# Kernel tuning notes

Measured on AMD Instinct MI355X. Metric: run time of the kernel, lower is better.

Reference implementation:

```python
import jax, jax.numpy as jnp
import numpy as np
from jax import lax

DIM = 512
E = 16
NC = 1000
ROUTER_TEMP = 1.0


def _conv(x, w, b):
    # NCHW conv, 3x3, SAME padding (matches nn.Conv2d(padding=1))
    y = lax.conv_general_dilated(x, w, (1, 1), 'SAME',
                                 dimension_numbers=('NCHW', 'OIHW', 'NCHW'))
    return y + b[None, :, None, None]


def _avgpool2(x):
    B, C, H, W = x.shape
    return x.reshape(B, C, H // 2, 2, W // 2, 2).mean(axis=(3, 5))


def setup_inputs() -> dict:
    key = jax.random.key(0)
    ks = jax.random.split(key, 12)
    B, C, H, W = 128, 3, 128, 128

    def init(k, shape, fan_in):
        return jax.random.normal(k, shape, jnp.float32) * (1.0 / np.sqrt(fan_in))

    return {
        'x': jax.random.normal(ks[0], (B, C, H, W), jnp.float32),
        'conv1_w': init(ks[1], (32, 3, 3, 3), 3 * 9),   'conv1_b': jnp.zeros((32,), jnp.float32),
        'conv2_w': init(ks[2], (32, 32, 3, 3), 32 * 9), 'conv2_b': jnp.zeros((32,), jnp.float32),
        'conv3_w': init(ks[3], (64, 32, 3, 3), 32 * 9), 'conv3_b': jnp.zeros((64,), jnp.float32),
        'conv4_w': init(ks[4], (64, 64, 3, 3), 64 * 9), 'conv4_b': jnp.zeros((64,), jnp.float32),
        'proj_w': init(ks[5], (64, DIM), 64),           'proj_b': jnp.zeros((DIM,), jnp.float32),
        'router_w': init(ks[6], (DIM, E), DIM),         'router_b': jnp.zeros((E,), jnp.float32),
        # stacked expert MLPs: Linear(dim,dim) -> ReLU -> Linear(dim,num_classes)
        'w1': init(ks[7], (E, DIM, DIM), DIM), 'b1': jnp.zeros((E, DIM), jnp.float32),
        'w2': init(ks[8], (E, DIM, NC), DIM),  'b2': jnp.zeros((E, NC), jnp.float32),
    }


def reference(x, conv1_w, conv1_b, conv2_w, conv2_b, conv3_w, conv3_b,
              conv4_w, conv4_b, proj_w, proj_b, router_w, router_b,
              w1, b1, w2, b2):
    # ---- Encoder ----
    h = jax.nn.relu(_conv(x, conv1_w, conv1_b))
    h = jax.nn.relu(_conv(h, conv2_w, conv2_b))
    h = _avgpool2(h)
    h = jax.nn.relu(_conv(h, conv3_w, conv3_b))
    h = _avgpool2(h)
    h = jax.nn.relu(_conv(h, conv4_w, conv4_b))
    h = h.mean(axis=(2, 3))                      # AdaptiveAvgPool2d(1) -> [B, 64]
    z = h @ proj_w + proj_b                      # [B, DIM]

    # ---- Router (top-1 gating) ----
    gate_logits = (z @ router_w + router_b) / ROUTER_TEMP   # [B, E]
    gate_probs = jax.nn.softmax(gate_logits, axis=-1)
    top1 = jnp.argmax(gate_probs, axis=-1)                  # [B] int
    B = z.shape[0]

    counts = lax.stop_gradient(
        jnp.zeros((E,), jnp.float32).at[top1].add(1.0) / B)
    importance = gate_probs.mean(axis=0)                    # [E]
    aux_loss = E * jnp.sum(counts * importance)

    # ---- Expert dispatch: gather per-token expert weights (top-1 hard routing) ----
    h1 = jax.nn.relu(jnp.einsum('bd,bdk->bk', z, w1[top1]) + b1[top1])   # [B, DIM]
    logits = jnp.einsum('bd,bdk->bk', h1, w2[top1]) + b2[top1]           # [B, NC]

    return logits, aux_loss, lax.stop_gradient(counts), lax.stop_gradient(importance)
```

## Files before the change

kernel.cpp:

```cpp
#include <hip/hip_runtime.h>
#include <math.h>

typedef unsigned short ushort_t;
typedef short short4x __attribute__((ext_vector_type(4)));
typedef short short8 __attribute__((ext_vector_type(8)));
typedef float f32x16 __attribute__((ext_vector_type(16)));

#define MFMA32(A,B,C) __builtin_amdgcn_mfma_f32_32x32x16_bf16(A,B,C,0,0,0)

__device__ __forceinline__ ushort_t f2bf(float f) {
    union { float f; unsigned u; } c; c.f = f;
    unsigned u = c.u;
    unsigned r = (u + 0x7FFFu + ((u >> 16) & 1u)) >> 16;
    return (ushort_t)r;
}

__device__ __forceinline__ unsigned pk2bf(float lo, float hi) {
    unsigned r;
    asm("v_cvt_pk_bf16_f32 %0, %1, %2" : "=v"(r) : "v"(lo), "v"(hi));
    return r;
}

__global__ __launch_bounds__(256) void k_wcvt(
    const float* __restrict__ c1w, const float* __restrict__ c2w,
    const float* __restrict__ c3w, const float* __restrict__ c4w,
    ushort_t* __restrict__ c1f, ushort_t* __restrict__ w2f,
    ushort_t* __restrict__ w3f, ushort_t* __restrict__ w4f,
    float* __restrict__ feat, float* __restrict__ tail)
{
    if (blockIdx.x == 33) {
        for (int i = threadIdx.x; i < 8192; i += 256) feat[i] = 0.f;
        if (threadIdx.x < 33) tail[threadIdx.x] = 0.f;
        return;
    }
    int r = blockIdx.x * 256 + threadIdx.x;
    int lane = r & 63, m = lane & 31, g = (lane >> 5) & 1;
    if (r < 1152) {
        int f = r >> 6, tau = f >> 1, h = f & 1, ky = tau / 3, kx = tau % 3;
        #pragma unroll
        for (int j = 0; j < 8; ++j) {
            int ic = h * 16 + g * 8 + j;
            w2f[r * 8 + j] = f2bf(c2w[((m * 32 + ic) * 3 + ky) * 3 + kx]);
        }
    } else if (r < 3456) {
        int rr = r - 1152;
        int f = rr >> 6;
        int ot = f / 18, fl = f % 18, tau = fl >> 1, h = fl & 1, ky = tau / 3, kx = tau % 3;
        int oc = ot * 32 + m;
        #pragma unroll
        for (int j = 0; j < 8; ++j) {
            int ic = h * 16 + g * 8 + j;
            w3f[rr * 8 + j] = f2bf(c3w[((oc * 32 + ic) * 3 + ky) * 3 + kx]);
        }
    } else if (r < 8064) {
        int rr = r - 3456;
        int f = rr >> 6;
        int ot = f / 36, fl = f % 36, tau = fl >> 2, h = fl & 3, ky = tau / 3, kx = tau % 3;
        int oc = ot * 32 + m;
        #pragma unroll
        for (int j = 0; j < 8; ++j) {
            int ic = h * 16 + g * 8 + j;
            w4f[rr * 8 + j] = f2bf(c4w[((oc * 64 + ic) * 3 + ky) * 3 + kx]);
        }
    } else if (r < 8256) {
        int rr = r - 8064;
        int f = rr >> 6;
        #pragma unroll
        for (int j = 0; j < 8; ++j) {
            int k = f * 16 + g * 8 + j;
            int p = k >> 2, c = k & 3;
            ushort_t v = 0;
            if (p < 9 && c < 3)
                v = f2bf(c1w[(m * 3 + c) * 9 + p]);
            c1f[rr * 8 + j] = v;
        }
    }
}

__global__ __launch_bounds__(512, 4) void k_c12(
    const float* __restrict__ x,
    const ushort_t* __restrict__ c1f, const float* __restrict__ c1b,
    const ushort_t* __restrict__ w2f, const float* __restrict__ c2b,
    ushort_t* __restrict__ a2, int zoff)
{
    __shared__ __align__(16) ushort_t xs[1600];
    __shared__ __align__(16) ushort_t a1s[324 * 40];
    __shared__ float c2bs[32], c1bs[32];
    const int t = threadIdx.x;
    const int bx = blockIdx.x, by = blockIdx.y, b = blockIdx.z + zoff;
    const int ox0 = bx * 16, oy0 = by * 16;

    if (t < 32) { c2bs[t] = c2b[t]; c1bs[t] = c1b[t]; }
    for (int i = t; i < 400; i += 512) {
        int yy = i / 20, xx = i % 20;
        int gy = oy0 - 2 + yy, gx = ox0 - 2 + xx;
        float v0 = 0.f, v1 = 0.f, v2 = 0.f;
        if (gy >= 0 && gy < 128 && gx >= 0 && gx < 128) {
            const float* px = x + ((size_t)(b * 3) * 128 + gy) * 128 + gx;
            v0 = px[0]; v1 = px[16384]; v2 = px[32768];
        }
        uint2 pk;
        pk.x = pk2bf(v0, v1);
        pk.y = pk2bf(v2, 0.f);
        *(uint2*)&xs[i * 4] = pk;
    }

    const int wave = t >> 6, lane = t & 63;
    const int n = lane & 31, g = lane >> 5;

    short8 a1f0 = *(const short8*)(c1f + lane * 8);
    short8 a1f1 = *(const short8*)(c1f + (64 + lane) * 8);
    short8 a1f2 = *(const short8*)(c1f + (128 + lane) * 8);
    __syncthreads();

    float cb1[16];
    #pragma unroll
    for (int qd = 0; qd < 4; ++qd)
        #pragma unroll
        for (int jj = 0; jj < 4; ++jj)
            cb1[qd * 4 + jj] = c1bs[qd * 8 + 4 * g + jj];

    for (int grp = wave; grp < 11; grp += 8) {
        int q = grp * 32 + n;
        bool qv = q < 324;
        int qc = qv ? q : 0;
        int cy = qc / 18, cx = qc % 18;
        int gy = oy0 - 1 + cy, gx = ox0 - 1 + cx;
        bool inimg = qv && gy >= 0 && gy < 128 && gx >= 0 && gx < 128;
        int base = (cy * 20 + cx) * 4;

        short4x q0 = *(const short4x*)&xs[base + (g ? 8 : 0)];
        short4x q1 = *(const short4x*)&xs[base + (g ? 80 : 4)];
        short4x q2 = *(const short4x*)&xs[base + (g ? 160 : 84)];
        short4x q3 = *(const short4x*)&xs[base + (g ? 164 : 88)];
        short4x q4 = *(const short4x*)&xs[base + 168];

        short8 b0 = __builtin_shufflevector(q0, q1, 0, 1, 2, 3, 4, 5, 6, 7);
        short8 b1 = __builtin_shufflevector(q2, q3, 0, 1, 2, 3, 4, 5, 6, 7);
        short8 b2 = __builtin_shufflevector(q4, q4, 0, 1, 2, 3, 0, 1, 2, 3);

        f32x16 acc;
        #pragma unroll
        for (int i = 0; i < 16; ++i) acc[i] = 0.f;
        acc = MFMA32(a1f0, b0, acc);
        acc = MFMA32(a1f1, b1, acc);
        acc = MFMA32(a1f2, b2, acc);

        if (qv) {
            ushort_t* dst = &a1s[q * 40 + 4 * g];
            #pragma unroll
            for (int qd = 0; qd < 4; ++qd) {
                float v0 = fmaxf(acc[qd * 4 + 0] + cb1[qd * 4 + 0], 0.f);
                float v1 = fmaxf(acc[qd * 4 + 1] + cb1[qd * 4 + 1], 0.f);
                float v2 = fmaxf(acc[qd * 4 + 2] + cb1[qd * 4 + 2], 0.f);
                float v3 = fmaxf(acc[qd * 4 + 3] + cb1[qd * 4 + 3], 0.f);
                uint2 pk;
                pk.x = inimg ? pk2bf(v0, v1) : 0u;
                pk.y = inimg ? pk2bf(v2, v3) : 0u;
                *(uint2*)&dst[8 * qd] = pk;
            }
        }
    }
    __syncthreads();

    const int ry = n >> 4, rx = n & 15;
    const int y2 = wave * 2 + ry;

    short8 af[18];
    #pragma unroll
    for (int f = 0; f < 18; ++f)
        af[f] = *(const short8*)(w2f + (f * 64 + lane) * 8);

    f32x16 acc;
    #pragma unroll
    for (int i = 0; i < 16; ++i) acc[i] = 0.f;

    #pragma unroll
    for (int tau = 0; tau < 9; ++tau) {
        int dy = tau / 3, dx = tau % 3;
        const ushort_t* bb = &a1s[((y2 + dy) * 18 + (rx + dx)) * 40 + g * 8];
        short8 b0 = *(const short8*)(bb);
        short8 b1 = *(const short8*)(bb + 16);
        acc = MFMA32(af[tau * 2 + 0], b0, acc);
        acc = MFMA32(af[tau * 2 + 1], b1, acc);
    }

    const int opy = by * 8 + wave;
    const int opx = bx * 8 + (rx >> 1);
    float pv[16];
    #pragma unroll
    for (int r = 0; r < 16; ++r) {
        float v = fmaxf(acc[r] + c2bs[(r & 3) + 8 * (r >> 2) + 4 * g], 0.f);
        v += __shfl_xor(v, 1);
        v += __shfl_xor(v, 16);
        pv[r] = v * 0.25f;
    }
    if ((lane & 17) == 0) {
        ushort_t* dst = &a2[(((size_t)b * 64 + opy) * 64 + opx) * 32 + 4 * g];
        #pragma unroll
        for (int qd = 0; qd < 4; ++qd) {
            uint2 pk;
            pk.x = pk2bf(pv[qd * 4 + 0], pv[qd * 4 + 1]);
            pk.y = pk2bf(pv[qd * 4 + 2], pv[qd * 4 + 3]);
            *(uint2*)&dst[8 * qd] = pk;
        }
    }
}

__global__ __launch_bounds__(512, 4) void k_c3(
    const ushort_t* __restrict__ a2, const ushort_t* __restrict__ w3f,
    const float* __restrict__ c3b, ushort_t* __restrict__ a3)
{
    __shared__ __align__(16) ushort_t s[324 * 40];
    __shared__ float bs[64];
    const int t = threadIdx.x;
    const int bx = blockIdx.x, by = blockIdx.y, b = blockIdx.z;
    const int x0 = bx * 16, y0 = by * 16;
    if (t < 64) bs[t] = c3b[t];
    for (int idx = t; idx < 1296; idx += 512) {
        int cell = idx >> 2, part = idx & 3;
        int cy = cell / 18, cx = cell % 18;
        int gy = y0 - 1 + cy, gx = x0 - 1 + cx;
        uint4 v = make_uint4(0, 0, 0, 0);
        if (gy >= 0 && gy < 64 && gx >= 0 && gx < 64)
            v = *(const uint4*)(a2 + (((size_t)b * 64 + gy) * 64 + gx) * 32 + part * 8);
        *(uint4*)(&s[cell * 40 + part * 8]) = v;
    }
    __syncthreads();

    const int wave = t >> 6, lane = t & 63;
    const int n = lane & 31, g = lane >> 5;
    const int ry = n >> 4, rx = n & 15;
    const int y3 = wave * 2 + ry;

    f32x16 acc0, acc1;
    #pragma unroll
    for (int i = 0; i < 16; ++i) { acc0[i] = 0.f; acc1[i] = 0.f; }

    #pragma unroll
    for (int tau = 0; tau < 9; ++tau) {
        int dy = tau / 3, dx = tau % 3;
        const ushort_t* bb = &s[((y3 + dy) * 18 + (rx + dx)) * 40 + g * 8];
        short8 b0 = *(const short8*)(bb);
        short8 b1 = *(const short8*)(bb + 16);
        short8 a00 = *(const short8*)(w3f + ((tau * 2 + 0) * 64 + lane) * 8);
        short8 a01 = *(const short8*)(w3f + ((tau * 2 + 1) * 64 + lane) * 8);
        short8 a10 = *(const short8*)(w3f + (((18 + tau * 2) + 0) * 64 + lane) * 8);
        short8 a11 = *(const short8*)(w3f + (((18 + tau * 2) + 1) * 64 + lane) * 8);
        acc0 = MFMA32(a00, b0, acc0);
        acc0 = MFMA32(a01, b1, acc0);
        acc1 = MFMA32(a10, b0, acc1);
        acc1 = MFMA32(a11, b1, acc1);
    }

    const int opy = by * 8 + wave;
    const int opx = bx * 8 + (rx >> 1);
    ushort_t* dst = &a3[(((size_t)b * 32 + opy) * 32 + opx) * 64 + 4 * g];
    #pragma unroll
    for (int ot = 0; ot < 2; ++ot) {
        const f32x16& ac = ot ? acc1 : acc0;
        float pv[16];
        #pragma unroll
        for (int r = 0; r < 16; ++r) {
            float v = fmaxf(ac[r] + bs[ot * 32 + (r & 3) + 8 * (r >> 2) + 4 * g], 0.f);
            v += __shfl_xor(v, 1);
            v += __shfl_xor(v, 16);
            pv[r] = v * 0.25f;
        }
        if ((lane & 17) == 0) {
            #pragma unroll
            for (int qd = 0; qd < 4; ++qd) {
                uint2 pk;
                pk.x = pk2bf(pv[qd * 4 + 0], pv[qd * 4 + 1]);
                pk.y = pk2bf(pv[qd * 4 + 2], pv[qd * 4 + 3]);
                *(uint2*)&dst[ot * 32 + 8 * qd] = pk;
            }
        }
    }
}

__global__ __launch_bounds__(512, 2) void k_c4(
    const ushort_t* __restrict__ a3, const ushort_t* __restrict__ w4f,
    const float* __restrict__ c4b, float* __restrict__ feat)
{
    __shared__ __align__(16) ushort_t s[324 * 72];
    __shared__ float bs[64];
    const int t = threadIdx.x;
    const int bx = blockIdx.x, by = blockIdx.y, b = blockIdx.z;
    const int x0 = bx * 16, y0 = by * 16;
    if (t < 64) bs[t] = c4b[t];
    for (int idx = t; idx < 2592; idx += 512) {
        int cell = idx >> 3, part = idx & 7;
        int cy = cell / 18, cx = cell % 18;
        int gy = y0 - 1 + cy, gx = x0 - 1 + cx;
        uint4 v = make_uint4(0, 0, 0, 0);
        if (gy >= 0 && gy < 32 && gx >= 0 && gx < 32)
            v = *(const uint4*)(a3 + (((size_t)b * 32 + gy) * 32 + gx) * 64 + part * 8);
        *(uint4*)(&s[cell * 72 + part * 8]) = v;
    }
    __syncthreads();

    const int wave = t >> 6, lane = t & 63;
    const int n = lane & 31, g = lane >> 5;
    const int ry = n >> 4, rx = n & 15;
    const int y4 = wave * 2 + ry;

    f32x16 acc0, acc1;
    #pragma unroll
    for (int i = 0; i < 16; ++i) { acc0[i] = 0.f; acc1[i] = 0.f; }

    #pragma unroll
    for (int hp = 0; hp < 2; ++hp) {
        #pragma unroll
        for (int tau = 0; tau < 9; ++tau) {
            int dy = tau / 3, dx = tau % 3;
            const ushort_t* bb = &s[((y4 + dy) * 18 + (rx + dx)) * 72 + hp * 32 + g * 8];
            short8 b0 = *(const short8*)(bb);
            short8 b1 = *(const short8*)(bb + 16);
            short8 a00 = *(const short8*)(w4f + ((tau * 4 + hp * 2 + 0) * 64 + lane) * 8);
            short8 a01 = *(const short8*)(w4f + ((tau * 4 + hp * 2 + 1) * 64 + lane) * 8);
            short8 a10 = *(const short8*)(w4f + ((36 + tau * 4 + hp * 2 + 0) * 64 + lane) * 8);
            short8 a11 = *(const short8*)(w4f + ((36 + tau * 4 + hp * 2 + 1) * 64 + lane) * 8);
            acc0 = MFMA32(a00, b0, acc0);
            acc0 = MFMA32(a01, b1, acc0);
            acc1 = MFMA32(a10, b0, acc1);
            acc1 = MFMA32(a11, b1, acc1);
        }
    }

    #pragma unroll
    for (int ot = 0; ot < 2; ++ot) {
        const f32x16& ac = ot ? acc1 : acc0;
        #pragma unroll
        for (int r = 0; r < 16; ++r) {
            int oc = ot * 32 + (r & 3) + 8 * (r >> 2) + 4 * g;
            float v = fmaxf(ac[r] + bs[oc], 0.f);
            v += __shfl_xor(v, 1);
            v += __shfl_xor(v, 2);
            v += __shfl_xor(v, 4);
            v += __shfl_xor(v, 8);
            v += __shfl_xor(v, 16);
            if ((lane & 31) == 0)
                atomicAdd(&feat[b * 64 + oc], v * (1.0f / 1024.0f));
        }
    }
}

__global__ __launch_bounds__(256) void k_router(
    const float* __restrict__ meanacc,
    const float* __restrict__ pw, const float* __restrict__ pb,
    const float* __restrict__ rw, const float* __restrict__ rb,
    ushort_t* __restrict__ zb, int* __restrict__ top1, float* __restrict__ tail)
{
    __shared__ float m[64];
    __shared__ float zs[512];
    __shared__ float part[256];
    __shared__ float gate[16];
    const int b = blockIdx.x, t = threadIdx.x;
    if (t < 64) m[t] = meanacc[b * 64 + t];
    __syncthreads();

    #pragma unroll
    for (int j = 0; j < 2; ++j) {
        int d = t + j * 256;
        float s = pb[d];
        for (int c = 0; c < 64; ++c) s += m[c] * pw[c * 512 + d];
        zs[d] = s;
        zb[b * 512 + d] = f2bf(s);
    }
    __syncthreads();
    {
        int e = t & 15, gg = t >> 4;
        float s = 0.f;
        for (int j = 0; j < 32; ++j) {
            int d = gg * 32 + j;
            s += zs[d] * rw[d * 16 + e];
        }
        part[t] = s;
    }
    __syncthreads();
    if (t < 16) {
        float s = rb[t];
        for (int gg = 0; gg < 16; ++gg) s += part[gg * 16 + t];
        gate[t] = s;
    }
    __syncthreads();
    if (t == 0) {
        float mx = gate[0];
        int am = 0;
        for (int e = 1; e < 16; ++e)
            if (gate[e] > mx) { mx = gate[e]; am = e; }
        float pr[16];
        float sum = 0.f;
        for (int e = 0; e < 16; ++e) { pr[e] = expf(gate[e] - mx); sum += pr[e]; }
        float inv = 1.f / sum;
        top1[b] = am;
        atomicAdd(&tail[1 + am], 1.0f / 128.0f);
        for (int e = 0; e < 16; ++e)
            atomicAdd(&tail[17 + e], pr[e] * inv * (1.0f / 128.0f));
    }
}

__global__ void k_sort(const int* __restrict__ top1, int* __restrict__ meta,
                       int* __restrict__ perm, float* __restrict__ tail)
{
    __shared__ int c[16], o[16], pos[128];
    const int t = threadIdx.x;
    if (t < 16) c[t] = 0;
    __syncthreads();
    int e = 0;
    if (t < 128) { e = top1[t]; pos[t] = atomicAdd(&c[e], 1); }
    __syncthreads();
    if (t == 0) {
        int s = 0;
        for (int i = 0; i < 16; ++i) { o[i] = s; s += c[i]; }
        int nt = 0;
        for (int i = 0; i < 16; ++i) {
            for (int r0 = 0; r0 < c[i]; r0 += 32) {
                meta[33 + nt] = i;
                meta[53 + nt] = o[i] + r0;
                int rem = c[i] - r0;
                meta[73 + nt] = rem < 32 ? rem : 32;
                ++nt;
            }
        }
        meta[32] = nt;
        for (int k = nt; k < 20; ++k) { meta[33 + k] = 0; meta[53 + k] = 0; meta[73 + k] = 0; }
        float s2 = 0.f;
        for (int i = 0; i < 16; ++i) s2 += tail[1 + i] * tail[17 + i];
        tail[0] = 16.0f * s2;
    }
    __syncthreads();
    if (t < 128) perm[o[e] + pos[t]] = t;
    if (t < 16) { meta[t] = c[t]; meta[16 + t] = o[t]; }
}

__global__ __launch_bounds__(64) void k_mlp1(
    const ushort_t* __restrict__ zb, const int* __restrict__ meta, const int* __restrict__ perm,
    const float* __restrict__ w1, const float* __restrict__ b1, ushort_t* __restrict__ h1b)
{
    const int ty = blockIdx.y;
    if (ty >= meta[32]) return;
    const int e = meta[33 + ty], ts = meta[53 + ty], rows = meta[73 + ty];
    const int n0 = blockIdx.x * 32;
    __shared__ __align__(16) ushort_t ws[32 * 520];
    __shared__ int tks[32];
    const int lane = threadIdx.x;
    const int mn = lane & 31, g = lane >> 5;

    if (lane < 32) tks[lane] = (lane < rows) ? perm[ts + lane] : -1;

    const float* Wg = w1 + ((size_t)e << 18) + n0;
    {
        const int cq = lane & 7, dg = lane >> 3;
        #pragma unroll 4
        for (int it = 0; it < 32; ++it) {
            int d = it * 16 + dg * 2;
            float4 va = *(const float4*)(Wg + (size_t)d * 512 + 4 * cq);
            float4 vb = *(const float4*)(Wg + (size_t)(d + 1) * 512 + 4 * cq);
            *(unsigned*)&ws[(4 * cq + 0) * 520 + d] = pk2bf(va.x, vb.x);
            *(unsigned*)&ws[(4 * cq + 1) * 520 + d] = pk2bf(va.y, vb.y);
            *(unsigned*)&ws[(4 * cq + 2) * 520 + d] = pk2bf(va.z, vb.z);
            *(unsigned*)&ws[(4 * cq + 3) * 520 + d] = pk2bf(va.w, vb.w);
        }
    }
    __syncthreads();

    const int tok_a = tks[mn] < 0 ? 0 : tks[mn];
    const ushort_t* za = zb + (size_t)tok_a * 512;

    f32x16 acc;
    #pragma unroll
    for (int i = 0; i < 16; ++i) acc[i] = 0.f;

    #pragma unroll 4
    for (int kt = 0; kt < 16; ++kt) {
        int k0 = kt * 32;
        short8 a0 = *(const short8*)(za + k0 + g * 8);
        short8 a1 = *(const short8*)(za + k0 + 16 + g * 8);
        short8 b0 = *(const short8*)(&ws[mn * 520 + k0 + g * 8]);
        short8 b1 = *(const short8*)(&ws[mn * 520 + k0 + 16 + g * 8]);
        acc = MFMA32(a0, b0, acc);
        acc = MFMA32(a1, b1, acc);
    }

    const float bias = b1[e * 512 + n0 + mn];
    #pragma unroll
    for (int r = 0; r < 16; ++r) {
        int mrow = (r & 3) + 8 * (r >> 2) + 4 * g;
        int tok = tks[mrow];
        if (tok >= 0) {
            float v = fmaxf(acc[r] + bias, 0.f);
            h1b[(size_t)tok * 512 + n0 + mn] = f2bf(v);
        }
    }
}

__global__ __launch_bounds__(64) void k_mlp2(
    const ushort_t* __restrict__ h1b, const int* __restrict__ meta, const int* __restrict__ perm,
    const float* __restrict__ w2, const float* __restrict__ b2, float* __restrict__ out)
{
    const int ty = blockIdx.y;
    if (ty >= meta[32]) return;
    const int e = meta[33 + ty], ts = meta[53 + ty], rows = meta[73 + ty];
    const int n0 = blockIdx.x * 32;
    __shared__ __align__(16) ushort_t ws[32 * 520];
    __shared__ int tks[32];
    const int lane = threadIdx.x;
    const int mn = lane & 31, g = lane >> 5;

    if (lane < 32) tks[lane] = (lane < rows) ? perm[ts + lane] : -1;

    const float* Wg = w2 + (size_t)e * 512000 + n0;
    {
        const int cq = lane & 7, dg = lane >> 3;
        const bool cut = (n0 == 992) && (cq >= 2);
        #pragma unroll 4
        for (int it = 0; it < 32; ++it) {
            int d = it * 16 + dg * 2;
            float4 va = make_float4(0.f, 0.f, 0.f, 0.f), vb = va;
            if (!cut) {
                va = *(const float4*)(Wg + (size_t)d * 1000 + 4 * cq);
                vb = *(const float4*)(Wg + (size_t)(d + 1) * 1000 + 4 * cq);
            }
            *(unsigned*)&ws[(4 * cq + 0) * 520 + d] = pk2bf(va.x, vb.x);
            *(unsigned*)&ws[(4 * cq + 1) * 520 + d] = pk2bf(va.y, vb.y);
            *(unsigned*)&ws[(4 * cq + 2) * 520 + d] = pk2bf(va.z, vb.z);
            *(unsigned*)&ws[(4 * cq + 3) * 520 + d] = pk2bf(va.w, vb.w);
        }
    }
    __syncthreads();

    const int tok_a = tks[mn] < 0 ? 0 : tks[mn];
    const ushort_t* ha = h1b + (size_t)tok_a * 512;

    f32x16 acc;
    #pragma unroll
    for (int i = 0; i < 16; ++i) acc[i] = 0.f;

    #pragma unroll 4
    for (int kt = 0; kt < 16; ++kt) {
        int k0 = kt * 32;
        short8 a0 = *(const short8*)(ha + k0 + g * 8);
        short8 a1 = *(const short8*)(ha + k0 + 16 + g * 8);
        short8 b0 = *(const short8*)(&ws[mn * 520 + k0 + g * 8]);
        short8 b1 = *(const short8*)(&ws[mn * 520 + k0 + 16 + g * 8]);
        acc = MFMA32(a0, b0, acc);
        acc = MFMA32(a1, b1, acc);
    }

    const int col = n0 + mn;
    if (col < 1000) {
        const float bias = b2[e * 1000 + col];
        #pragma unroll
        for (int r = 0; r < 16; ++r) {
            int mrow = (r & 3) + 8 * (r >> 2) + 4 * g;
            int tok = tks[mrow];
            if (tok >= 0)
                out[(size_t)tok * 1000 + col] = acc[r] + bias;
        }
    }
}

extern "C" void kernel_launch(void* const* d_in, const int* in_sizes, int n_in,
                              void* d_out, int out_size, void* d_ws, size_t ws_size,
                              hipStream_t stream)
{
    const float* x   = (const float*)d_in[0];
    const float* c1w = (const float*)d_in[1];
    const float* c1b = (const float*)d_in[2];
    const float* c2w = (const float*)d_in[3];
    const float* c2b = (const float*)d_in[4];
    const float* c3w = (const float*)d_in[5];
    const float* c3b = (const float*)d_in[6];
    const float* c4w = (const float*)d_in[7];
    const float* c4b = (const float*)d_in[8];
    const float* pw  = (const float*)d_in[9];
    const float* pb  = (const float*)d_in[10];
    const float* rw  = (const float*)d_in[11];
    const float* rb  = (const float*)d_in[12];
    const float* w1  = (const float*)d_in[13];
    const float* b1  = (const float*)d_in[14];
    const float* w2  = (const float*)d_in[15];
    const float* b2  = (const float*)d_in[16];

    float* out = (float*)d_out;
    float* tail = out + 128000;

    char* w = (char*)d_ws;
    ushort_t* a2   = (ushort_t*)(w);
    ushort_t* a3   = (ushort_t*)(w + 33554432);
    ushort_t* w2f  = (ushort_t*)(w + 50331648);
    ushort_t* w3f  = (ushort_t*)(w + 50350080);
    ushort_t* w4f  = (ushort_t*)(w + 50386944);
    ushort_t* c1f  = (ushort_t*)(w + 50460672);
    float*    feat = (float*)(w + 50464768);
    ushort_t* zb   = (ushort_t*)(w + 50497536);
    ushort_t* h1b  = (ushort_t*)(w + 50628608);
    int*      top1 = (int*)(w + 50759680);
    int*      meta = (int*)(w + 50760192);
    int*      perm = (int*)(w + 50760704);

    k_wcvt  <<<34, 256, 0, stream>>>(c1w, c2w, c3w, c4w, c1f, w2f, w3f, w4f, feat, tail);
    k_c12   <<<dim3(8, 8, 64), 512, 0, stream>>>(x, c1f, c1b, w2f, c2b, a2, 0);
    k_c12   <<<dim3(8, 8, 64), 512, 0, stream>>>(x, c1f, c1b, w2f, c2b, a2, 64);
    k_c3    <<<dim3(4, 4, 128), 512, 0, stream>>>(a2, w3f, c3b, a3);
    k_c4    <<<dim3(2, 2, 128), 512, 0, stream>>>(a3, w4f, c4b, feat);
    k_router<<<128, 256, 0, stream>>>(feat, pw, pb, rw, rb, zb, top1, tail);
    k_sort  <<<1, 128, 0, stream>>>(top1, meta, perm, tail);
    k_mlp1  <<<dim3(16, 20), 64, 0, stream>>>(zb, meta, perm, w1, b1, h1b);
    k_mlp2  <<<dim3(32, 20), 64, 0, stream>>>(h1b, meta, perm, w2, b2, out);
}
```

Measured before the change: 206.1 us.

## Switch conv2-4 to 16x16x32 MFMA with pool-grouped pixel mapping

Reworks the conv2, conv3 and conv4 inner loops to use the 16x16x32 bf16 MFMA with activations as the A operand and repacked weights as B. Rows are mapped so each group of four rows is one 2x2 pooling window, which lets pooling be done in registers without cross-lane shuffles. Conv4 now reduces into shared memory before a single global atomic per channel, and its occupancy bound is raised from 2 to 4. The two half-batch conv1/2 launches are merged into one. The trade-off is more MFMA instructions with fewer cycles each, plus narrower per-element global stores.

```diff
diff --git a/kernel.cpp b/kernel.cpp
--- a/kernel.cpp
+++ b/kernel.cpp
@@ -4,9 +4,11 @@
 typedef unsigned short ushort_t;
 typedef short short4x __attribute__((ext_vector_type(4)));
 typedef short short8 __attribute__((ext_vector_type(8)));
+typedef float f32x4 __attribute__((ext_vector_type(4)));
 typedef float f32x16 __attribute__((ext_vector_type(16)));
 
 #define MFMA32(A,B,C) __builtin_amdgcn_mfma_f32_32x32x16_bf16(A,B,C,0,0,0)
+#define MFMA16(A,B,C) __builtin_amdgcn_mfma_f32_16x16x32_bf16(A,B,C,0,0,0)
 
 __device__ __forceinline__ ushort_t f2bf(float f) {
     union { float f; unsigned u; } c; c.f = f;
@@ -34,40 +36,41 @@
         return;
     }
     int r = blockIdx.x * 256 + threadIdx.x;
-    int lane = r & 63, m = lane & 31, g = (lane >> 5) & 1;
-    if (r < 1152) {
-        int f = r >> 6, tau = f >> 1, h = f & 1, ky = tau / 3, kx = tau % 3;
+    int f = r >> 6, lane = r & 63;
+    int col = lane & 15, kg = lane >> 4;
+    if (f < 18) {
+        int tau = f >> 1, ocg = f & 1;
+        int oc = ocg * 16 + col;
         #pragma unroll
         for (int j = 0; j < 8; ++j) {
-            int ic = h * 16 + g * 8 + j;
-            w2f[r * 8 + j] = f2bf(c2w[((m * 32 + ic) * 3 + ky) * 3 + kx]);
-        }
-    } else if (r < 3456) {
-        int rr = r - 1152;
-        int f = rr >> 6;
-        int ot = f / 18, fl = f % 18, tau = fl >> 1, h = fl & 1, ky = tau / 3, kx = tau % 3;
-        int oc = ot * 32 + m;
+            int ic = kg * 8 + j;
+            w2f[r * 8 + j] = f2bf(c2w[(oc * 32 + ic) * 9 + tau]);
+        }
+    } else if (f < 54) {
+        int rr = f - 18;
+        int tau = rr >> 2, ocg = rr & 3;
+        int oc = ocg * 16 + col;
         #pragma unroll
         for (int j = 0; j < 8; ++j) {
-            int ic = h * 16 + g * 8 + j;
-            w3f[rr * 8 + j] = f2bf(c3w[((oc * 32 + ic) * 3 + ky) * 3 + kx]);
-        }
-    } else if (r < 8064) {
-        int rr = r - 3456;
-        int f = rr >> 6;
-        int ot = f / 36, fl = f % 36, tau = fl >> 2, h = fl & 3, ky = tau / 3, kx = tau % 3;
-        int oc = ot * 32 + m;
+            int ic = kg * 8 + j;
+            w3f[(r - 18 * 64) * 8 + j] = f2bf(c3w[(oc * 32 + ic) * 9 + tau]);
+        }
+    } else if (f < 126) {
+        int rr = f - 54;
+        int q = rr >> 2, ocg = rr & 3, tau = q >> 1, ks = q & 1;
+        int oc = ocg * 16 + col;
         #pragma unroll
         for (int j = 0; j < 8; ++j) {
-            int ic = h * 16 + g * 8 + j;
-            w4f[rr * 8 + j] = f2bf(c4w[((oc * 64 + ic) * 3 + ky) * 3 + kx]);
-        }
-    } else if (r < 8256) {
-        int rr = r - 8064;
-        int f = rr >> 6;
+            int ic = ks * 32 + kg * 8 + j;
+            w4f[(r - 54 * 64) * 8 + j] = f2bf(c4w[(oc * 64 + ic) * 9 + tau]);
+        }
+    } else if (f < 129) {
+        int rr = r - 126 * 64;
+        int f1 = rr >> 6;
+        int m = lane & 31, g = (lane >> 5) & 1;
         #pragma unroll
         for (int j = 0; j < 8; ++j) {
-            int k = f * 16 + g * 8 + j;
+            int k = f1 * 16 + g * 8 + j;
             int p = k >> 2, c = k & 3;
             ushort_t v = 0;
             if (p < 9 && c < 3)
@@ -81,13 +84,13 @@
     const float* __restrict__ x,
     const ushort_t* __restrict__ c1f, const float* __restrict__ c1b,
     const ushort_t* __restrict__ w2f, const float* __restrict__ c2b,
-    ushort_t* __restrict__ a2, int zoff)
+    ushort_t* __restrict__ a2)
 {
     __shared__ __align__(16) ushort_t xs[1600];
     __shared__ __align__(16) ushort_t a1s[324 * 40];
     __shared__ float c2bs[32], c1bs[32];
     const int t = threadIdx.x;
-    const int bx = blockIdx.x, by = blockIdx.y, b = blockIdx.z + zoff;
+    const int bx = blockIdx.x, by = blockIdx.y, b = blockIdx.z;
     const int ox0 = bx * 16, oy0 = by * 16;
 
     if (t < 32) { c2bs[t] = c2b[t]; c1bs[t] = c1b[t]; }
@@ -163,47 +166,33 @@
     }
     __syncthreads();
 
-    const int ry = n >> 4, rx = n & 15;
-    const int y2 = wave * 2 + ry;
-
-    short8 af[18];
-    #pragma unroll
-    for (int f = 0; f < 18; ++f)
-        af[f] = *(const short8*)(w2f + (f * 64 + lane) * 8);
-
-    f32x16 acc;
-    #pragma unroll
-    for (int i = 0; i < 16; ++i) acc[i] = 0.f;
-
-    #pragma unroll
-    for (int tau = 0; tau < 9; ++tau) {
-        int dy = tau / 3, dx = tau % 3;
-        const ushort_t* bb = &a1s[((y2 + dy) * 18 + (rx + dx)) * 40 + g * 8];
-        short8 b0 = *(const short8*)(bb);
-        short8 b1 = *(const short8*)(bb + 16);
-        acc = MFMA32(af[tau * 2 + 0], b0, acc);
-        acc = MFMA32(af[tau * 2 + 1], b1, acc);
-    }
-
-    const int opy = by * 8 + wave;
-    const int opx = bx * 8 + (rx >> 1);
-    float pv[16];
-    #pragma unroll
-    for (int r = 0; r < 16; ++r) {
-        float v = fmaxf(acc[r] + c2bs[(r & 3) + 8 * (r >> 2) + 4 * g], 0.f);
-        v += __shfl_xor(v, 1);
-        v += __shfl_xor(v, 16);
-        pv[r] = v * 0.25f;
-    }
-    if ((lane & 17) == 0) {
-        ushort_t* dst = &a2[(((size_t)b * 64 + opy) * 64 + opx) * 32 + 4 * g];
-        #pragma unroll
-        for (int qd = 0; qd < 4; ++qd) {
-            uint2 pk;
-            pk.x = pk2bf(pv[qd * 4 + 0], pv[qd * 4 + 1]);
-            pk.y = pk2bf(pv[qd * 4 + 2], pv[qd * 4 + 3]);
-            *(uint2*)&dst[8 * qd] = pk;
-        }
+    const int col = lane & 15, kg = lane >> 4;
+    const float bias0 = c2bs[col], bias1 = c2bs[16 + col];
+    #pragma unroll
+    for (int i = 0; i < 2; ++i) {
+        const int pg = wave * 2 + i;
+        const int qiA = pg * 4 + (col >> 2), subA = col & 3;
+        const int y2 = (qiA >> 3) * 2 + (subA >> 1);
+        const int x2 = (qiA & 7) * 2 + (subA & 1);
+        const ushort_t* abase = &a1s[(y2 * 18 + x2) * 40 + kg * 8];
+        f32x4 acc0 = {0.f, 0.f, 0.f, 0.f}, acc1 = {0.f, 0.f, 0.f, 0.f};
+        #pragma unroll
+        for (int tau = 0; tau < 9; ++tau) {
+            short8 a = *(const short8*)(abase + ((tau / 3) * 18 + (tau % 3)) * 40);
+            short8 w0 = *(const short8*)(w2f + ((tau * 2 + 0) * 64 + lane) * 8);
+            short8 w1 = *(const short8*)(w2f + ((tau * 2 + 1) * 64 + lane) * 8);
+            acc0 = MFMA16(a, w0, acc0);
+            acc1 = MFMA16(a, w1, acc1);
+        }
+        const int qo = pg * 4 + kg;
+        const int poy = by * 8 + (qo >> 3), pox = bx * 8 + (qo & 7);
+        float s0 = fmaxf(acc0[0] + bias0, 0.f) + fmaxf(acc0[1] + bias0, 0.f)
+                 + fmaxf(acc0[2] + bias0, 0.f) + fmaxf(acc0[3] + bias0, 0.f);
+        float s1 = fmaxf(acc1[0] + bias1, 0.f) + fmaxf(acc1[1] + bias1, 0.f)
+                 + fmaxf(acc1[2] + bias1, 0.f) + fmaxf(acc1[3] + bias1, 0.f);
+        ushort_t* dst = &a2[(((size_t)b * 64 + poy) * 64 + pox) * 32];
+        dst[col] = f2bf(s0 * 0.25f);
+        dst[16 + col] = f2bf(s1 * 0.25f);
     }
 }
 
@@ -229,66 +218,53 @@
     __syncthreads();
 
     const int wave = t >> 6, lane = t & 63;
-    const int n = lane & 31, g = lane >> 5;
-    const int ry = n >> 4, rx = n & 15;
-    const int y3 = wave * 2 + ry;
-
-    f32x16 acc0, acc1;
-    #pragma unroll
-    for (int i = 0; i < 16; ++i) { acc0[i] = 0.f; acc1[i] = 0.f; }
-
-    #pragma unroll
-    for (int tau = 0; tau < 9; ++tau) {
-        int dy = tau / 3, dx = tau % 3;
-        const ushort_t* bb = &s[((y3 + dy) * 18 + (rx + dx)) * 40 + g * 8];
-        short8 b0 = *(const short8*)(bb);
-        short8 b1 = *(const short8*)(bb + 16);
-        short8 a00 = *(const short8*)(w3f + ((tau * 2 + 0) * 64 + lane) * 8);
-        short8 a01 = *(const short8*)(w3f + ((tau * 2 + 1) * 64 + lane) * 8);
-        short8 a10 = *(const short8*)(w3f + (((18 + tau * 2) + 0) * 64 + lane) * 8);
-        short8 a11 = *(const short8*)(w3f + (((18 + tau * 2) + 1) * 64 + lane) * 8);
-        acc0 = MFMA32(a00, b0, acc0);
-        acc0 = MFMA32(a01, b1, acc0);
-        acc1 = MFMA32(a10, b0, acc1);
-        acc1 = MFMA32(a11, b1, acc1);
-    }
-
-    const int opy = by * 8 + wave;
-    const int opx = bx * 8 + (rx >> 1);
-    ushort_t* dst = &a3[(((size_t)b * 32 + opy) * 32 + opx) * 64 + 4 * g];
-    #pragma unroll
-    for (int ot = 0; ot < 2; ++ot) {
-        const f32x16& ac = ot ? acc1 : acc0;
-        float pv[16];
-        #pragma unroll
-        for (int r = 0; r < 16; ++r) {
-            float v = fmaxf(ac[r] + bs[ot * 32 + (r & 3) + 8 * (r >> 2) + 4 * g], 0.f);
-            v += __shfl_xor(v, 1);
-            v += __shfl_xor(v, 16);
-            pv[r] = v * 0.25f;
-        }
-        if ((lane & 17) == 0) {
+    const int col = lane & 15, kg = lane >> 4;
+    float bias[4];
+    #pragma unroll
+    for (int ocg = 0; ocg < 4; ++ocg) bias[ocg] = bs[ocg * 16 + col];
+
+    #pragma unroll
+    for (int i = 0; i < 2; ++i) {
+        const int pg = wave * 2 + i;
+        const int qiA = pg * 4 + (col >> 2), subA = col & 3;
+        const int y3 = (qiA >> 3) * 2 + (subA >> 1);
+        const int x3 = (qiA & 7) * 2 + (subA & 1);
+        const ushort_t* abase = &s[(y3 * 18 + x3) * 40 + kg * 8];
+        f32x4 acc[4];
+        #pragma unroll
+        for (int ocg = 0; ocg < 4; ++ocg) acc[ocg] = f32x4{0.f, 0.f, 0.f, 0.f};
+        #pragma unroll
+        for (int tau = 0; tau < 9; ++tau) {
+            short8 a = *(const short8*)(abase + ((tau / 3) * 18 + (tau % 3)) * 40);
             #pragma unroll
-            for (int qd = 0; qd < 4; ++qd) {
-                uint2 pk;
-                pk.x = pk2bf(pv[qd * 4 + 0], pv[qd * 4 + 1]);
-                pk.y = pk2bf(pv[qd * 4 + 2], pv[qd * 4 + 3]);
-                *(uint2*)&dst[ot * 32 + 8 * qd] = pk;
+            for (int ocg = 0; ocg < 4; ++ocg) {
+                short8 wv = *(const short8*)(w3f + ((tau * 4 + ocg) * 64 + lane) * 8);
+                acc[ocg] = MFMA16(a, wv, acc[ocg]);
             }
         }
-    }
-}
-
-__global__ __launch_bounds__(512, 2) void k_c4(
+        const int qo = pg * 4 + kg;
+        const int poy = by * 8 + (qo >> 3), pox = bx * 8 + (qo & 7);
+        ushort_t* dst = &a3[(((size_t)b * 32 + poy) * 32 + pox) * 64];
+        #pragma unroll
+        for (int ocg = 0; ocg < 4; ++ocg) {
+            float sv = fmaxf(acc[ocg][0] + bias[ocg], 0.f) + fmaxf(acc[ocg][1] + bias[ocg], 0.f)
+                     + fmaxf(acc[ocg][2] + bias[ocg], 0.f) + fmaxf(acc[ocg][3] + bias[ocg], 0.f);
+            dst[ocg * 16 + col] = f2bf(sv * 0.25f);
+        }
+    }
+}
+
+__global__ __launch_bounds__(512, 4) void k_c4(
     const ushort_t* __restrict__ a3, const ushort_t* __restrict__ w4f,
     const float* __restrict__ c4b, float* __restrict__ feat)
 {
     __shared__ __align__(16) ushort_t s[324 * 72];
     __shared__ float bs[64];
+    __shared__ float fp[64];
     const int t = threadIdx.x;
     const int bx = blockIdx.x, by = blockIdx.y, b = blockIdx.z;
     const int x0 = bx * 16, y0 = by * 16;
-    if (t < 64) bs[t] = c4b[t];
+    if (t < 64) { bs[t] = c4b[t]; fp[t] = 0.f; }
     for (int idx = t; idx < 2592; idx += 512) {
         int cell = idx >> 3, part = idx & 7;
         int cy = cell / 18, cx = cell % 18;
@@ -301,49 +277,48 @@
     __syncthreads();
 
     const int wave = t >> 6, lane = t & 63;
-    const int n = lane & 31, g = lane >> 5;
-    const int ry = n >> 4, rx = n & 15;
-    const int y4 = wave * 2 + ry;
-
-    f32x16 acc0, acc1;
-    #pragma unroll
-    for (int i = 0; i < 16; ++i) { acc0[i] = 0.f; acc1[i] = 0.f; }
-
-    #pragma unroll
-    for (int hp = 0; hp < 2; ++hp) {
+    const int col = lane & 15, kg = lane >> 4;
+    float bias[4], fpart[4] = {0.f, 0.f, 0.f, 0.f};
+    #pragma unroll
+    for (int ocg = 0; ocg < 4; ++ocg) bias[ocg] = bs[ocg * 16 + col];
+
+    #pragma unroll
+    for (int i = 0; i < 2; ++i) {
+        const int pg = wave * 2 + i;
+        const int qiA = pg * 4 + (col >> 2), subA = col & 3;
+        const int y4 = (qiA >> 3) * 2 + (subA >> 1);
+        const int x4 = (qiA & 7) * 2 + (subA & 1);
+        const ushort_t* abase = &s[(y4 * 18 + x4) * 72 + kg * 8];
+        f32x4 acc[4];
+        #pragma unroll
+        for (int ocg = 0; ocg < 4; ++ocg) acc[ocg] = f32x4{0.f, 0.f, 0.f, 0.f};
         #pragma unroll
         for (int tau = 0; tau < 9; ++tau) {
-            int dy = tau / 3, dx = tau % 3;
-            const ushort_t* bb = &s[((y4 + dy) * 18 + (rx + dx)) * 72 + hp * 32 + g * 8];
-            short8 b0 = *(const short8*)(bb);
-            short8 b1 = *(const short8*)(bb + 16);
-            short8 a00 = *(const short8*)(w4f + ((tau * 4 + hp * 2 + 0) * 64 + lane) * 8);
-            short8 a01 = *(const short8*)(w4f + ((tau * 4 + hp * 2 + 1) * 64 + lane) * 8);
-            short8 a10 = *(const short8*)(w4f + ((36 + tau * 4 + hp * 2 + 0) * 64 + lane) * 8);
-            short8 a11 = *(const short8*)(w4f + ((36 + tau * 4 + hp * 2 + 1) * 64 + lane) * 8);
-            acc0 = MFMA32(a00, b0, acc0);
-            acc0 = MFMA32(a01, b1, acc0);
-            acc1 = MFMA32(a10, b0, acc1);
-            acc1 = MFMA32(a11, b1, acc1);
-        }
-    }
-
-    #pragma unroll
-    for (int ot = 0; ot < 2; ++ot) {
-        const f32x16& ac = ot ? acc1 : acc0;
-        #pragma unroll
-        for (int r = 0; r < 16; ++r) {
-            int oc = ot * 32 + (r & 3) + 8 * (r >> 2) + 4 * g;
-            float v = fmaxf(ac[r] + bs[oc], 0.f);
-            v += __shfl_xor(v, 1);
-            v += __shfl_xor(v, 2);
-            v += __shfl_xor(v, 4);
-            v += __shfl_xor(v, 8);
-            v += __shfl_xor(v, 16);
-            if ((lane & 31) == 0)
-                atomicAdd(&feat[b * 64 + oc], v * (1.0f / 1024.0f));
-        }
-    }
+            #pragma unroll
+            for (int ks = 0; ks < 2; ++ks) {
+                short8 a = *(const short8*)(abase + ((tau / 3) * 18 + (tau % 3)) * 72 + ks * 32);
+                #pragma unroll
+                for (int ocg = 0; ocg < 4; ++ocg) {
+                    short8 wv = *(const short8*)(w4f + (((tau * 2 + ks) * 4 + ocg) * 64 + lane) * 8);
+                    acc[ocg] = MFMA16(a, wv, acc[ocg]);
+                }
+            }
+        }
+        #pragma unroll
+        for (int ocg = 0; ocg < 4; ++ocg) {
+            fpart[ocg] += fmaxf(acc[ocg][0] + bias[ocg], 0.f) + fmaxf(acc[ocg][1] + bias[ocg], 0.f)
+                        + fmaxf(acc[ocg][2] + bias[ocg], 0.f) + fmaxf(acc[ocg][3] + bias[ocg], 0.f);
+        }
+    }
+    #pragma unroll
+    for (int ocg = 0; ocg < 4; ++ocg) {
+        float v = fpart[ocg];
+        v += __shfl_xor(v, 16);
+        v += __shfl_xor(v, 32);
+        if (lane < 16) atomicAdd(&fp[ocg * 16 + col], v);
+    }
+    __syncthreads();
+    if (t < 64) atomicAdd(&feat[b * 64 + t], fp[t] * (1.0f / 1024.0f));
 }
 
 __global__ __launch_bounds__(256) void k_router(
@@ -549,15 +524,15 @@
         acc = MFMA32(a1, b1, acc);
     }
 
-    const int col = n0 + mn;
-    if (col < 1000) {
-        const float bias = b2[e * 1000 + col];
+    const int colo = n0 + mn;
+    if (colo < 1000) {
+        const float bias = b2[e * 1000 + colo];
         #pragma unroll
         for (int r = 0; r < 16; ++r) {
             int mrow = (r & 3) + 8 * (r >> 2) + 4 * g;
             int tok = tks[mrow];
             if (tok >= 0)
-                out[(size_t)tok * 1000 + col] = acc[r] + bias;
+                out[(size_t)tok * 1000 + colo] = acc[r] + bias;
         }
     }
 }
@@ -602,8 +577,7 @@
     int*      perm = (int*)(w + 50760704);
 
     k_wcvt  <<<34, 256, 0, stream>>>(c1w, c2w, c3w, c4w, c1f, w2f, w3f, w4f, feat, tail);
-    k_c12   <<<dim3(8, 8, 64), 512, 0, stream>>>(x, c1f, c1b, w2f, c2b, a2, 0);
-    k_c12   <<<dim3(8, 8, 64), 512, 0, stream>>>(x, c1f, c1b, w2f, c2b, a2, 64);
+    k_c12   <<<dim3(8, 8, 128), 512, 0, stream>>>(x, c1f, c1b, w2f, c2b, a2);
     k_c3    <<<dim3(4, 4, 128), 512, 0, stream>>>(a2, w3f, c3b, a3);
     k_c4    <<<dim3(2, 2, 128), 512, 0, stream>>>(a3, w4f, c4b, feat);
     k_router<<<128, 256, 0, stream>>>(feat, pw, pb, rw, rb, zb, top1, tail);
```

Measured after the change: 212.3 us, median of 2. +3.0%, slower.
